# Optimization experiments

Measured on AMD Instinct MI355X. Metric: run time of the kernel, lower is better.

## Reference

```python
import jax, jax.numpy as jnp
import numpy as np

GAMMA = 2.0
CONTEXT_WINDOW = 100


def setup_inputs() -> dict:
    key = jax.random.key(0)
    k1, k2 = jax.random.split(key)
    B, S, C = 64, 131072, 3
    inputs = jax.random.normal(k1, (B, S, C), dtype=jnp.float32)
    targets = jax.random.randint(k2, (B, S), 0, C, dtype=jnp.int32)
    alpha = jnp.array([0.25, 1.0, 1.0], dtype=jnp.float32)
    return {"inputs": inputs, "targets": targets, "alpha": alpha}


def _window_mask(targets, window):
    # mask[b, i] = True iff any positive target within +/- window of i;
    # rows with no positives are fully True (matches torch loop semantics).
    B, S = targets.shape
    pos = targets > 0                                   # (B, S) bool
    cs = jnp.cumsum(pos.astype(jnp.int32), axis=1)      # inclusive prefix sums
    c = jnp.concatenate([jnp.zeros((B, 1), jnp.int32), cs], axis=1)  # (B, S+1)
    idx = jnp.arange(S)
    hi = jnp.minimum(idx + window + 1, S)               # exclusive end
    lo = jnp.maximum(idx - window, 0)                   # inclusive start
    count = c[:, hi] - c[:, lo]                         # positives in window
    mask = count > 0
    has_pos = pos.any(axis=1, keepdims=True)
    return jnp.where(has_pos, mask, True)


def reference(inputs, targets, alpha):
    # inputs: (B, S, C) logits; targets: (B, S) class indices
    mask = _window_mask(targets, CONTEXT_WINDOW)                     # (B, S)
    logp = jax.nn.log_softmax(inputs, axis=-1)                       # (B, S, C)
    ce = -jnp.take_along_axis(logp, targets[..., None].astype(jnp.int32), axis=-1)[..., 0]
    p_t = jnp.exp(-ce)
    focal = alpha[targets] * (1.0 - p_t) ** GAMMA * ce               # (B, S)
    m = mask.astype(inputs.dtype)
    # masked mean == mean over selected elements in the torch version
    return jnp.sum(focal * m) / jnp.sum(m)
```

## Files before the change

### kernel.cpp

```cpp
#include <hip/hip_runtime.h>

#define BB 64
#define SS 131072
#define WIN 100
#define TILE 4096
#define NTHREADS 256
#define TILES_PER_ROW (SS / TILE)
#define NBLOCKS (BB * TILES_PER_ROW)
#define EXT (TILE + 2*WIN)
#define NWORDS ((EXT + 63) / 64)
#define SH_BYTES (NWORDS * 64)
#define K4TOT (SH_BYTES / 4)
#define SROUNDS ((K4TOT + NTHREADS - 1) / NTHREADS)
#define NGROUPS 4

typedef float  fx4 __attribute__((ext_vector_type(4)));
typedef int    ix4 __attribute__((ext_vector_type(4)));

__global__ __launch_bounds__(NTHREADS, 8) void focal_main(
    const float* __restrict__ inputs, const int* __restrict__ targets,
    const float* __restrict__ alpha, double* __restrict__ slots)
{
    __shared__ __align__(16) unsigned char sh_t[SH_BYTES];
    __shared__ unsigned long long wbits[NWORDS];
    __shared__ unsigned long long mbits[NWORDS];
    __shared__ fx4 in_lds[NTHREADS * 3];
    __shared__ double red[(NTHREADS/64) * 4];

    const int t = threadIdx.x;
    const int b = blockIdx.x / TILES_PER_ROW;
    const int tile = blockIdx.x % TILES_PER_ROW;
    const int s0 = tile * TILE;
    const int ext_lo = (s0 - WIN > 0) ? (s0 - WIN) : 0;
    const int ext_hi = (s0 + TILE + WIN < SS) ? (s0 + TILE + WIN) : SS;
    const int ext_len = ext_hi - ext_lo;
    const int tr_lo = s0 - ext_lo;

    const int* trow = targets + (long)b * SS;
    #pragma unroll
    for (int it = 0; it < SROUNDS; ++it) {
        const int k4 = it * NTHREADS + t;
        if (k4 < K4TOT) {
            unsigned int pk = 0;
            if (4 * k4 < ext_len) {
                const ix4 tv4 =
                    __builtin_nontemporal_load((const ix4*)(trow + ext_lo + 4 * k4));
                pk = (unsigned)(tv4.x & 3) | ((unsigned)(tv4.y & 3) << 8) |
                     ((unsigned)(tv4.z & 3) << 16) | ((unsigned)(tv4.w & 3) << 24);
            }
            ((unsigned int*)sh_t)[k4] = pk;
        }
    }
    __syncthreads();

    int cnt_p = 0;
    if (t < NWORDS) {
        const uint4* qp = (const uint4*)(sh_t + (t << 6));
        unsigned long long wv = 0;
        #pragma unroll
        for (int r = 0; r < 4; ++r) {
            const uint4 u = qp[r];
            unsigned int x, nz;
            x = u.x; nz = (x | (x >> 1)) & 0x01010101u;
            wv |= (unsigned long long)((nz * 0x01020408u) >> 24) << (r*16 + 0);
            x = u.y; nz = (x | (x >> 1)) & 0x01010101u;
            wv |= (unsigned long long)((nz * 0x01020408u) >> 24) << (r*16 + 4);
            x = u.z; nz = (x | (x >> 1)) & 0x01010101u;
            wv |= (unsigned long long)((nz * 0x01020408u) >> 24) << (r*16 + 8);
            x = u.w; nz = (x | (x >> 1)) & 0x01010101u;
            wv |= (unsigned long long)((nz * 0x01020408u) >> 24) << (r*16 + 12);
        }
        wbits[t] = wv;
        int lo_bit = tr_lo - (t << 6);        if (lo_bit < 0) lo_bit = 0;
        int hi_bit = tr_lo + TILE - (t << 6); if (hi_bit > 64) hi_bit = 64;
        if (hi_bit > lo_bit) {
            unsigned long long rm = (hi_bit >= 64) ? ~0ULL : ((1ULL << hi_bit) - 1);
            rm &= (~0ULL << lo_bit);
            cnt_p = __popcll(wv & rm);
        }
    }
    __syncthreads();

    if (t < NWORDS) {
        const unsigned long long a = (t >= 2) ? wbits[t-2] : 0ULL;
        const unsigned long long bw = (t >= 1) ? wbits[t-1] : 0ULL;
        const unsigned long long c = wbits[t];
        const unsigned long long d = (t+1 < NWORDS) ? wbits[t+1] : 0ULL;
        const unsigned long long e = (t+2 < NWORDS) ? wbits[t+2] : 0ULL;
        unsigned long long m = c ? ~0ULL : 0ULL;
        if (d) { const int lo = __builtin_ctzll(d) - 36;
                 m |= (lo <= 0) ? ~0ULL : (~0ULL << lo); }
        if (e) { const int lo = __builtin_ctzll(e) + 28;
                 if (lo <= 63) m |= (~0ULL << lo); }
        if (bw) { const int hi = 63 - __builtin_clzll(bw) + 36;
                  m |= (hi >= 63) ? ~0ULL : (~0ULL >> (63 - hi)); }
        if (a) { const int hi = 63 - __builtin_clzll(a) - 28;
                 if (hi >= 0) m |= (hi >= 63) ? ~0ULL : (~0ULL >> (63 - hi)); }
        mbits[t] = m;
    }
    __syncthreads();

    const float a0 = alpha[0], a1 = alpha[1], a2 = alpha[2];
    const float* inrow = inputs + (long)b * SS * 3;
    float fsum_m = 0.0f, fsum_a = 0.0f;
    int cnt_m = 0;

    #pragma unroll
    for (int g = 0; g < NGROUPS; ++g) {
        const fx4* gsrc = (const fx4*)(inrow + (long)(s0 + g * 1024) * 3);
        const fx4 v0 = __builtin_nontemporal_load(gsrc + t);
        const fx4 v1 = __builtin_nontemporal_load(gsrc + NTHREADS + t);
        const fx4 v2 = __builtin_nontemporal_load(gsrc + 2 * NTHREADS + t);
        in_lds[t] = v0;
        in_lds[NTHREADS + t] = v1;
        in_lds[2 * NTHREADS + t] = v2;
        __syncthreads();

        const fx4* my = (const fx4*)((const float*)in_lds + t * 12);
        const fx4 c0 = my[0], c1 = my[1], c2 = my[2];

        const int p = s0 + g * 1024 + t * 4;
        const int j0 = p - ext_lo;
        const unsigned long long mw = mbits[j0 >> 6];
        const unsigned int tpack = *(const unsigned int*)(sh_t + j0);
        const float xs[12] = {c0.x, c0.y, c0.z, c0.w, c1.x, c1.y, c1.z, c1.w,
                              c2.x, c2.y, c2.z, c2.w};
        #pragma unroll
        for (int j = 0; j < 4; ++j) {
            const float x0 = xs[3*j], x1 = xs[3*j+1], x2 = xs[3*j+2];
            const int tv = (tpack >> (8 * j)) & 0xFF;
            const float mx = fmaxf(x0, fmaxf(x1, x2));
            const float e0 = __expf(x0 - mx), e1 = __expf(x1 - mx), e2 = __expf(x2 - mx);
            const float sum = e0 + e1 + e2;
            const float xt  = (tv == 0) ? x0 : ((tv == 1) ? x1 : x2);
            const float et  = (tv == 0) ? e0 : ((tv == 1) ? e1 : e2);
            const float ce  = __logf(sum) + (mx - xt);
            const float pt  = et * __frcp_rn(sum);
            const float w   = (tv == 0) ? a0 : ((tv == 1) ? a1 : a2);
            const float om  = 1.0f - pt;
            const float focal = w * om * om * ce;
            const bool  m   = (mw >> ((j0 & 63) + j)) & 1ULL;

            fsum_a += focal;
            fsum_m += m ? focal : 0.0f;
            cnt_m  += m ? 1 : 0;
        }
        __syncthreads();
    }

    const int wave = t >> 6, lane = t & 63;
    #pragma unroll
    for (int off = 32; off >= 1; off >>= 1) {
        fsum_m += __shfl_down(fsum_m, off);
        fsum_a += __shfl_down(fsum_a, off);
        cnt_m  += __shfl_down(cnt_m, off);
        cnt_p  += __shfl_down(cnt_p, off);
    }
    if (lane == 0) {
        red[wave*4]   = (double)fsum_m; red[wave*4+1] = (double)cnt_m;
        red[wave*4+2] = (double)fsum_a; red[wave*4+3] = (double)cnt_p;
    }
    __syncthreads();
    if (t == 0) {
        double sm = 0, sc = 0, sa = 0, sp = 0;
        #pragma unroll
        for (int w = 0; w < NTHREADS/64; ++w) {
            sm += red[w*4]; sc += red[w*4+1]; sa += red[w*4+2]; sp += red[w*4+3];
        }
        double* slot = slots + (long)blockIdx.x * 4;
        slot[0] = sm;
        slot[1] = sc;
        slot[2] = sa;
        slot[3] = sp;
    }
}

__global__ __launch_bounds__(NTHREADS) void focal_final(
    const double* __restrict__ slots, float* __restrict__ out)
{
    __shared__ double red[(NTHREADS/64) * 2];
    __shared__ double tot[2];
    const int t = threadIdx.x;
    const int wave = t >> 6, lane = t & 63;

    double sm = 0.0, sc = 0.0;
    for (int k = t; k < NBLOCKS; k += NTHREADS) {
        sm += slots[(long)k * 4 + 0];
        sc += slots[(long)k * 4 + 1];
    }
    #pragma unroll
    for (int off = 32; off >= 1; off >>= 1) {
        sm += __shfl_down(sm, off);
        sc += __shfl_down(sc, off);
    }
    if (lane == 0) { red[wave*2] = sm; red[wave*2+1] = sc; }
    __syncthreads();
    if (t == 0) {
        double a = 0, b = 0;
        #pragma unroll
        for (int w = 0; w < NTHREADS/64; ++w) { a += red[w*2]; b += red[w*2+1]; }
        tot[0] = a; tot[1] = b;
    }
    __syncthreads();

    double corr_s = 0.0, corr_c = 0.0;
    if (t < BB) {
        double row_sum = 0.0, row_pos = 0.0;
        for (int j = 0; j < TILES_PER_ROW; ++j) {
            const long blk = (long)t * TILES_PER_ROW + j;
            row_sum += slots[blk * 4 + 2];
            row_pos += slots[blk * 4 + 3];
        }
        if (row_pos == 0.0) { corr_s = row_sum; corr_c = (double)SS; }
    }
    if (wave == 0) {
        #pragma unroll
        for (int off = 32; off >= 1; off >>= 1) {
            corr_s += __shfl_down(corr_s, off);
            corr_c += __shfl_down(corr_c, off);
        }
        if (t == 0) {
            const double total = tot[0] + corr_s;
            const double count = tot[1] + corr_c;
            out[0] = (float)(total / count);
        }
    }
}

extern "C" void kernel_launch(void* const* d_in, const int* in_sizes, int n_in,
                              void* d_out, int out_size, void* d_ws, size_t ws_size,
                              hipStream_t stream) {
    const float* inputs  = (const float*)d_in[0];
    const int*   targets = (const int*)d_in[1];
    const float* alpha   = (const float*)d_in[2];
    float* out = (float*)d_out;

    double* slots = (double*)d_ws;

    focal_main<<<NBLOCKS, NTHREADS, 0, stream>>>(inputs, targets, alpha, slots);
    focal_final<<<1, NTHREADS, 0, stream>>>(slots, out);
}
```

Measured before the change: 167.7 us.

## Double-buffer logit tiles in LDS with register prefetch and reduce exp count

The logits for the first group are now loaded before the targets and mask phase, and the group loop uses two LDS buffers with the next group's loads already in flight. This lets global-memory latency overlap with mask construction and the focal computation, and removes one barrier per iteration. The softmax now sorts the three logits so that only two exponentials are evaluated, since the max term is exactly 1. In exchange, the prefetch registers and the doubled LDS buffer raise resource use, and the launch-bounds occupancy hint drops from 8 to 5.

```diff
diff --git a/kernel.cpp b/kernel.cpp
--- a/kernel.cpp
+++ b/kernel.cpp
@@ -13,18 +13,19 @@
 #define K4TOT (SH_BYTES / 4)
 #define SROUNDS ((K4TOT + NTHREADS - 1) / NTHREADS)
 #define NGROUPS 4
+#define GF4 (NTHREADS * 3)
 
 typedef float  fx4 __attribute__((ext_vector_type(4)));
 typedef int    ix4 __attribute__((ext_vector_type(4)));
 
-__global__ __launch_bounds__(NTHREADS, 8) void focal_main(
+__global__ __launch_bounds__(NTHREADS, 5) void focal_main(
     const float* __restrict__ inputs, const int* __restrict__ targets,
     const float* __restrict__ alpha, double* __restrict__ slots)
 {
     __shared__ __align__(16) unsigned char sh_t[SH_BYTES];
     __shared__ unsigned long long wbits[NWORDS];
     __shared__ unsigned long long mbits[NWORDS];
-    __shared__ fx4 in_lds[NTHREADS * 3];
+    __shared__ fx4 buf[2][GF4];
     __shared__ double red[(NTHREADS/64) * 4];
 
     const int t = threadIdx.x;
@@ -35,6 +36,12 @@
     const int ext_hi = (s0 + TILE + WIN < SS) ? (s0 + TILE + WIN) : SS;
     const int ext_len = ext_hi - ext_lo;
     const int tr_lo = s0 - ext_lo;
+
+    const float* inrow = inputs + (long)b * SS * 3;
+    const fx4* gbase = (const fx4*)(inrow + (long)s0 * 3);
+    fx4 q0 = __builtin_nontemporal_load(gbase + t);
+    fx4 q1 = __builtin_nontemporal_load(gbase + NTHREADS + t);
+    fx4 q2 = __builtin_nontemporal_load(gbase + 2 * NTHREADS + t);
 
     const int* trow = targets + (long)b * SS;
     #pragma unroll
@@ -100,24 +107,35 @@
     }
     __syncthreads();
 
+    buf[0][t] = q0; buf[0][NTHREADS + t] = q1; buf[0][2*NTHREADS + t] = q2;
+    {
+        const fx4* g1src = (const fx4*)(inrow + (long)(s0 + 1024) * 3);
+        q0 = __builtin_nontemporal_load(g1src + t);
+        q1 = __builtin_nontemporal_load(g1src + NTHREADS + t);
+        q2 = __builtin_nontemporal_load(g1src + 2 * NTHREADS + t);
+    }
+    __syncthreads();
+
     const float a0 = alpha[0], a1 = alpha[1], a2 = alpha[2];
-    const float* inrow = inputs + (long)b * SS * 3;
     float fsum_m = 0.0f, fsum_a = 0.0f;
     int cnt_m = 0;
 
     #pragma unroll
     for (int g = 0; g < NGROUPS; ++g) {
-        const fx4* gsrc = (const fx4*)(inrow + (long)(s0 + g * 1024) * 3);
-        const fx4 v0 = __builtin_nontemporal_load(gsrc + t);
-        const fx4 v1 = __builtin_nontemporal_load(gsrc + NTHREADS + t);
-        const fx4 v2 = __builtin_nontemporal_load(gsrc + 2 * NTHREADS + t);
-        in_lds[t] = v0;
-        in_lds[NTHREADS + t] = v1;
-        in_lds[2 * NTHREADS + t] = v2;
-        __syncthreads();
-
-        const fx4* my = (const fx4*)((const float*)in_lds + t * 12);
+        const fx4* my = (const fx4*)((const float*)buf[g & 1] + t * 12);
         const fx4 c0 = my[0], c1 = my[1], c2 = my[2];
+
+        if (g + 1 < NGROUPS) {
+            buf[(g+1) & 1][t] = q0;
+            buf[(g+1) & 1][NTHREADS + t] = q1;
+            buf[(g+1) & 1][2*NTHREADS + t] = q2;
+        }
+        if (g + 2 < NGROUPS) {
+            const fx4* gn = (const fx4*)(inrow + (long)(s0 + (g+2) * 1024) * 3);
+            q0 = __builtin_nontemporal_load(gn + t);
+            q1 = __builtin_nontemporal_load(gn + NTHREADS + t);
+            q2 = __builtin_nontemporal_load(gn + 2 * NTHREADS + t);
+        }
 
         const int p = s0 + g * 1024 + t * 4;
         const int j0 = p - ext_lo;
@@ -130,10 +148,13 @@
             const float x0 = xs[3*j], x1 = xs[3*j+1], x2 = xs[3*j+2];
             const int tv = (tpack >> (8 * j)) & 0xFF;
             const float mx = fmaxf(x0, fmaxf(x1, x2));
-            const float e0 = __expf(x0 - mx), e1 = __expf(x1 - mx), e2 = __expf(x2 - mx);
-            const float sum = e0 + e1 + e2;
+            const float mn = fminf(x0, fminf(x1, x2));
+            const float md = fmaxf(fminf(x0, x1), fminf(fmaxf(x0, x1), x2));
+            const float emd = __expf(md - mx);
+            const float emn = __expf(mn - mx);
+            const float sum = 1.0f + emd + emn;
             const float xt  = (tv == 0) ? x0 : ((tv == 1) ? x1 : x2);
-            const float et  = (tv == 0) ? e0 : ((tv == 1) ? e1 : e2);
+            const float et  = (xt == mx) ? 1.0f : ((xt == md) ? emd : emn);
             const float ce  = __logf(sum) + (mx - xt);
             const float pt  = et * __frcp_rn(sum);
             const float w   = (tv == 0) ? a0 : ((tv == 1) ? a1 : a2);
@@ -145,7 +166,7 @@
             fsum_m += m ? focal : 0.0f;
             cnt_m  += m ? 1 : 0;
         }
-        __syncthreads();
+        if (g + 1 < NGROUPS) __syncthreads();
     }
 
     const int wave = t >> 6, lane = t & 63;
```

Measured after the change: 167.6 us. About the same (-0.0%).
